# Kernel optimization log

Hardware: AMD Instinct MI355X
Metric: run time of the kernel (lower is better)

Reference implementation:

```python
import jax, jax.numpy as jnp
import numpy as np

TEMPERATURE = 0.07
NORM_EPS = 1e-12  # matches torch F.normalize eps


def setup_inputs() -> dict:
    key = jax.random.key(0)
    k1, k2 = jax.random.split(key)
    emb = jax.random.normal(k1, (4, 256, 61, 61), dtype=jnp.float32)
    targets = jax.random.randint(k2, (4, 61, 61), 0, 5, dtype=jnp.int64)
    return {"emb": emb, "targets": targets}


def reference(emb, targets):
    n, c, h, w = emb.shape
    # (N,C,H,W) -> (N*H*W, C), L2-normalized per pixel
    feats = emb.transpose(0, 2, 3, 1).reshape(-1, c)
    norms = jnp.maximum(jnp.linalg.norm(feats, axis=1, keepdims=True), NORM_EPS)
    feats = feats / norms
    labels = targets.reshape(-1)  # (T,)
    T = labels.shape[0]

    sim = jnp.matmul(feats, feats.T) / TEMPERATURE  # (T,T)
    exp_sim = jnp.exp(sim)

    eye = jnp.eye(T, dtype=bool)
    pos_mask = (labels[None, :] == labels[:, None]) & ~eye  # (T,T) bool

    sum_pos = jnp.sum(jnp.where(pos_mask, exp_sim, 0.0), axis=1)  # (T,)
    sum_all = exp_sim.sum(axis=1) - jnp.exp(jnp.diagonal(sim))    # (T,)

    valid = sum_pos > 0
    # safe log: substitute 1.0 where invalid to avoid -inf/NaN, then mask
    safe_pos = jnp.where(valid, sum_pos, 1.0)
    safe_all = jnp.where(valid, sum_all, 1.0)
    per_row = jnp.where(valid, -(jnp.log(safe_pos) - jnp.log(safe_all)), 0.0)
    loss = per_row.sum() / jnp.maximum(valid.sum(), 1).astype(per_row.dtype)
    return loss
```

## Files before the change

kernel.cpp:

```cpp
#include <hip/hip_runtime.h>
#include <cstdint>
#include <cstddef>

#define T_REAL 14884
#define TPAD   14976
#define CDIM   256
#define HW     3721
#define NTILE  234
#define NRB    117
#define NSLICE 8

static constexpr float SCALE = 20.6099291555566f;

typedef _Float16 f16x8 __attribute__((ext_vector_type(8)));
typedef float    f32x4 __attribute__((ext_vector_type(4)));

#define OFF_FEATS 0u
#define SZ_FEATS  ((unsigned)TPAD * CDIM * 2u)
#define OFF_SUMSQ (OFF_FEATS + SZ_FEATS)
#define OFF_LAB   (OFF_SUMSQ + 65536u)
#define OFF_PART  (OFF_LAB + 65536u)
#define SZ_PART   ((unsigned)NRB * NSLICE * 128u * 2u * 4u)
#define OFF_ACC   (OFF_PART + SZ_PART)

__global__ void k_init(const int* __restrict__ targets, int* __restrict__ labels,
                       _Float16* __restrict__ feats, float* __restrict__ sumsq,
                       float* __restrict__ accum) {
    int t = blockIdx.x * 256 + threadIdx.x;
    if (t == 0) { accum[0] = 0.f; accum[1] = 0.f; }
    if (t < TPAD) {
        labels[t] = (t < T_REAL) ? targets[t] : -1;
        if (t < T_REAL) {
            sumsq[t] = 0.f;
        } else {
            float4 z = make_float4(0.f, 0.f, 0.f, 0.f);
            float4* row = (float4*)(feats + (size_t)t * CDIM);
#pragma unroll
            for (int q = 0; q < 32; ++q) row[q] = z;
        }
    }
}

__global__ void k_norm(const float* __restrict__ emb, float* __restrict__ sumsq) {
    int hw = blockIdx.x * 256 + threadIdx.x;
    int n  = blockIdx.y, cq = blockIdx.z;
    if (hw >= HW) return;
    const float* p = emb + ((size_t)(n * CDIM + cq * 64)) * HW + hw;
    float s = 0.f;
#pragma unroll 16
    for (int c = 0; c < 64; ++c) { float v = p[(size_t)c * HW]; s += v * v; }
    atomicAdd(&sumsq[n * HW + hw], s);
}

__global__ void k_pack(const float* __restrict__ emb, const float* __restrict__ sumsq,
                       _Float16* __restrict__ feats) {
    __shared__ float tile[64][65];
    int tx = threadIdx.x & 63, ty = threadIdx.x >> 6;
    int hw0 = blockIdx.x * 64, c0 = blockIdx.y * 64, n = blockIdx.z;
#pragma unroll
    for (int it = 0; it < 16; ++it) {
        int cl = it * 4 + ty;
        int hw = hw0 + tx;
        float v = 0.f;
        if (hw < HW) v = emb[((size_t)(n * CDIM + c0 + cl)) * HW + hw];
        tile[cl][tx] = v;
    }
    __syncthreads();
#pragma unroll
    for (int it = 0; it < 16; ++it) {
        int pl = it * 4 + ty;
        int hw = hw0 + pl;
        if (hw < HW) {
            int t = n * HW + hw;
            float inv = 1.f / fmaxf(sqrtf(sumsq[t]), 1e-12f);
            feats[(size_t)t * CDIM + c0 + tx] = (_Float16)(tile[tx][pl] * inv);
        }
    }
}

__device__ __forceinline__ void stage_tile(const _Float16* __restrict__ feats, int jbase,
                                           _Float16* bufp, int tid) {
#pragma unroll
    for (int sweep = 0; sweep < 4; ++sweep) {
        int ch = sweep * 512 + tid;
        int j  = ch >> 5;
        int qs = ch & 31;
        int qsrc = qs ^ (j & 7);
        const _Float16* src = feats + ((size_t)(jbase + j)) * CDIM + qsrc * 8;
        __builtin_amdgcn_global_load_lds(
            (const __attribute__((address_space(1))) void*)src,
            (__attribute__((address_space(3))) void*)(bufp + (size_t)ch * 8),
            16, 0, 0);
    }
}

__global__ __launch_bounds__(512, 4) void k_main(const _Float16* __restrict__ feats,
                                                 const int* __restrict__ labels,
                                                 float* __restrict__ partials) {
    __shared__ _Float16 buf[2][64 * 256];
    const int tid  = threadIdx.x;
    const int wave = tid >> 6, lane = tid & 63;
    const int il   = lane & 15, quad = lane >> 4;
    const int rb = blockIdx.x, slice = blockIdx.y;
    const int i = rb * 128 + wave * 16 + il;
    const int lab_i = labels[i];

    f16x8 bfr[8];
    const _Float16* fi = feats + (size_t)i * CDIM;
#pragma unroll
    for (int ks = 0; ks < 8; ++ks)
        bfr[ks] = *reinterpret_cast<const f16x8*>(fi + ks * 32 + quad * 8);

    const int hb = (il >> 2) & 1;
    const int qx = quad ^ (il & 3);
    int lofs[4];
#pragma unroll
    for (int jj = 0; jj < 4; ++jj) lofs[jj] = (jj * 16 + il) * 256 + qx * 8;

    float accA = 0.f, accP = 0.f;

    stage_tile(feats, slice * 64, &buf[0][0], tid);
    int cur = 0;
    for (int jt = slice; jt < NTILE; jt += NSLICE) {
        asm volatile("s_waitcnt vmcnt(0)\n\ts_barrier" ::: "memory");
        int nxt = jt + NSLICE;
        if (nxt < NTILE) stage_tile(feats, nxt * 64, &buf[cur ^ 1][0], tid);

        const _Float16* bufc = &buf[cur][0];
        f32x4 acc[4];
#pragma unroll
        for (int jj = 0; jj < 4; ++jj) acc[jj] = (f32x4){0.f, 0.f, 0.f, 0.f};

#pragma unroll
        for (int ks = 0; ks < 8; ++ks) {
            const int ksx = ks ^ hb;
#pragma unroll
            for (int jj = 0; jj < 4; ++jj) {
                f16x8 a = *reinterpret_cast<const f16x8*>(bufc + lofs[jj] + ksx * 32);
                acc[jj] = __builtin_amdgcn_mfma_f32_16x16x32_f16(a, bfr[ks], acc[jj], 0, 0, 0);
            }
        }

        const int jb = jt * 64;
#pragma unroll
        for (int jj = 0; jj < 4; ++jj) {
            const int4 lj = *reinterpret_cast<const int4*>(&labels[jb + jj * 16 + quad * 4]);
#pragma unroll
            for (int r = 0; r < 4; ++r) {
                int ljr = (r == 0) ? lj.x : (r == 1) ? lj.y : (r == 2) ? lj.z : lj.w;
                float e  = exp2f(acc[jj][r] * SCALE);
                float ev = (ljr >= 0) ? e : 0.f;
                accA += ev;
                accP += (ljr == lab_i) ? ev : 0.f;
            }
        }
        cur ^= 1;
    }

    float nsq = 0.f;
#pragma unroll
    for (int ks = 0; ks < 8; ++ks)
#pragma unroll
        for (int e = 0; e < 8; ++e) { float x = (float)bfr[ks][e]; nsq += x * x; }
    nsq += __shfl_xor(nsq, 16);
    nsq += __shfl_xor(nsq, 32);

    accA += __shfl_xor(accA, 16); accA += __shfl_xor(accA, 32);
    accP += __shfl_xor(accP, 16); accP += __shfl_xor(accP, 32);

    if ((((rb * 2 + (wave >> 2)) & 7)) == slice) {
        float ed = exp2f(nsq * SCALE);
        accA -= ed; accP -= ed;
    }

    if (quad == 0) {
        int idx = ((rb * NSLICE + slice) * 128 + wave * 16 + il) * 2;
        partials[idx]     = accA;
        partials[idx + 1] = accP;
    }
}

__global__ void k_reduce(const float* __restrict__ partials, float* __restrict__ accum) {
    int rb = blockIdx.x;
    int tl = threadIdx.x;
    int t  = rb * 128 + tl;
    float per = 0.f, cnt = 0.f;
    if (t < T_REAL) {
        float sA = 0.f, sP = 0.f;
#pragma unroll
        for (int s = 0; s < NSLICE; ++s) {
            int idx = ((rb * NSLICE + s) * 128 + tl) * 2;
            sA += partials[idx];
            sP += partials[idx + 1];
        }
        if (sP > 0.f) {
            per = logf(sA) - logf(sP);
            cnt = 1.f;
        }
    }
#pragma unroll
    for (int off = 32; off >= 1; off >>= 1) {
        per += __shfl_xor(per, off);
        cnt += __shfl_xor(cnt, off);
    }
    if ((tl & 63) == 0) { atomicAdd(&accum[0], per); atomicAdd(&accum[1], cnt); }
}

__global__ void k_final(const float* __restrict__ accum, float* __restrict__ out) {
    out[0] = accum[0] / fmaxf(accum[1], 1.0f);
}

extern "C" void kernel_launch(void* const* d_in, const int* in_sizes, int n_in,
                              void* d_out, int out_size, void* d_ws, size_t ws_size,
                              hipStream_t stream) {
    const float* emb     = (const float*)d_in[0];
    const int*   targets = (const int*)d_in[1];
    float*       out     = (float*)d_out;
    char*        ws      = (char*)d_ws;

    _Float16* feats    = (_Float16*)(ws + OFF_FEATS);
    float*    sumsq    = (float*)(ws + OFF_SUMSQ);
    int*      labels   = (int*)(ws + OFF_LAB);
    float*    partials = (float*)(ws + OFF_PART);
    float*    accum    = (float*)(ws + OFF_ACC);

    k_init  <<<dim3(59),        dim3(256), 0, stream>>>(targets, labels, feats, sumsq, accum);
    k_norm  <<<dim3(15, 4, 4),  dim3(256), 0, stream>>>(emb, sumsq);
    k_pack  <<<dim3(59, 4, 4),  dim3(256), 0, stream>>>(emb, sumsq, feats);
    k_main  <<<dim3(NRB, NSLICE), dim3(512), 0, stream>>>(feats, labels, partials);
    k_reduce<<<dim3(NRB),       dim3(128), 0, stream>>>(partials, accum);
    k_final <<<dim3(1),         dim3(1),   0, stream>>>(accum, out);
}
```

Baseline: 265.8 us.

## Use 32x32 MFMA 64-row register tiles, fuse norm+pack, fold scale into features

The main kernel switches to 32x32x16 MFMAs, with each wave holding 64 query rows in registers, so each LDS tile is reused across more rows. The padding becomes a multiple of 512, and slices go from 8 to 16. The norm and pack kernels are merged into one prep kernel that computes the sum of squares in LDS, removing the atomics and an extra pass over the embeddings. The sqrt of the temperature/log2e scale is folded into the stored features, and padding columns are no longer masked; their exp(0) contributions are subtracted as a constant in the reduction. The cost is fp16 features with scaled magnitudes and higher register pressure (launch bounds lowered to 2).

```diff
diff --git a/kernel.cpp b/kernel.cpp
--- a/kernel.cpp
+++ b/kernel.cpp
@@ -3,36 +3,42 @@
 #include <cstddef>
 
 #define T_REAL 14884
-#define TPAD   14976
+#define TPAD   15360
 #define CDIM   256
 #define HW     3721
-#define NTILE  234
-#define NRB    117
-#define NSLICE 8
-
-static constexpr float SCALE = 20.6099291555566f;
-
-typedef _Float16 f16x8 __attribute__((ext_vector_type(8)));
-typedef float    f32x4 __attribute__((ext_vector_type(4)));
+#define NRB    30
+#define NCT    240
+#define NSL    16
+#define TPS    15
+#define NPADJ  476.0f
+
+static constexpr float SQRT_SCALE = 4.53981598f;
+
+typedef _Float16 f16x8  __attribute__((ext_vector_type(8)));
+typedef float    f32x16 __attribute__((ext_vector_type(16)));
+
+__device__ __forceinline__ float exp2_fast(float x) {
+#if __has_builtin(__builtin_amdgcn_exp2f)
+    return __builtin_amdgcn_exp2f(x);
+#else
+    return exp2f(x);
+#endif
+}
 
 #define OFF_FEATS 0u
 #define SZ_FEATS  ((unsigned)TPAD * CDIM * 2u)
-#define OFF_SUMSQ (OFF_FEATS + SZ_FEATS)
-#define OFF_LAB   (OFF_SUMSQ + 65536u)
-#define OFF_PART  (OFF_LAB + 65536u)
-#define SZ_PART   ((unsigned)NRB * NSLICE * 128u * 2u * 4u)
+#define OFF_LAB   (OFF_FEATS + SZ_FEATS)
+#define OFF_PART  (OFF_LAB + (unsigned)TPAD * 4u)
+#define SZ_PART   ((unsigned)NRB * NSL * 512u * 8u)
 #define OFF_ACC   (OFF_PART + SZ_PART)
 
 __global__ void k_init(const int* __restrict__ targets, int* __restrict__ labels,
-                       _Float16* __restrict__ feats, float* __restrict__ sumsq,
-                       float* __restrict__ accum) {
+                       _Float16* __restrict__ feats, float* __restrict__ accum) {
     int t = blockIdx.x * 256 + threadIdx.x;
     if (t == 0) { accum[0] = 0.f; accum[1] = 0.f; }
     if (t < TPAD) {
         labels[t] = (t < T_REAL) ? targets[t] : -1;
-        if (t < T_REAL) {
-            sumsq[t] = 0.f;
-        } else {
+        if (t >= T_REAL) {
             float4 z = make_float4(0.f, 0.f, 0.f, 0.f);
             float4* row = (float4*)(feats + (size_t)t * CDIM);
 #pragma unroll
@@ -41,39 +47,38 @@
     }
 }
 
-__global__ void k_norm(const float* __restrict__ emb, float* __restrict__ sumsq) {
-    int hw = blockIdx.x * 256 + threadIdx.x;
-    int n  = blockIdx.y, cq = blockIdx.z;
-    if (hw >= HW) return;
-    const float* p = emb + ((size_t)(n * CDIM + cq * 64)) * HW + hw;
-    float s = 0.f;
-#pragma unroll 16
-    for (int c = 0; c < 64; ++c) { float v = p[(size_t)c * HW]; s += v * v; }
-    atomicAdd(&sumsq[n * HW + hw], s);
-}
-
-__global__ void k_pack(const float* __restrict__ emb, const float* __restrict__ sumsq,
-                       _Float16* __restrict__ feats) {
-    __shared__ float tile[64][65];
-    int tx = threadIdx.x & 63, ty = threadIdx.x >> 6;
-    int hw0 = blockIdx.x * 64, c0 = blockIdx.y * 64, n = blockIdx.z;
-#pragma unroll
-    for (int it = 0; it < 16; ++it) {
-        int cl = it * 4 + ty;
-        int hw = hw0 + tx;
-        float v = 0.f;
-        if (hw < HW) v = emb[((size_t)(n * CDIM + c0 + cl)) * HW + hw];
-        tile[cl][tx] = v;
-    }
+__global__ void k_prep(const float* __restrict__ emb, _Float16* __restrict__ feats) {
+    __shared__ float tile[64][257];
+    __shared__ float sspart[4][64];
+    const int tid = threadIdx.x;
+    const int lane = tid & 63, w = tid >> 6;
+    const int px0 = blockIdx.x * 64, n = blockIdx.y;
+    const int hw = px0 + lane;
+
+    float ssq = 0.f;
+    for (int ci = w; ci < CDIM; ci += 4) {
+        float v = (hw < HW) ? emb[((size_t)(n * CDIM + ci)) * HW + hw] : 0.f;
+        tile[lane][ci] = v;
+        ssq += v * v;
+    }
+    sspart[w][lane] = ssq;
     __syncthreads();
-#pragma unroll
-    for (int it = 0; it < 16; ++it) {
-        int pl = it * 4 + ty;
-        int hw = hw0 + pl;
-        if (hw < HW) {
-            int t = n * HW + hw;
-            float inv = 1.f / fmaxf(sqrtf(sumsq[t]), 1e-12f);
-            feats[(size_t)t * CDIM + c0 + tx] = (_Float16)(tile[tx][pl] * inv);
+
+    const int p = tid >> 2, q = tid & 3;
+    float s = sspart[q][p];
+    s += __shfl_xor(s, 1);
+    s += __shfl_xor(s, 2);
+    float inv = SQRT_SCALE / fmaxf(sqrtf(s), 1e-12f);
+
+    const int hwp = px0 + p;
+    if (hwp < HW) {
+        _Float16* dst = feats + ((size_t)(n * HW + hwp)) * CDIM + q * 64;
+#pragma unroll
+        for (int g = 0; g < 8; ++g) {
+            f16x8 o;
+#pragma unroll
+            for (int e = 0; e < 8; ++e) o[e] = (_Float16)(tile[p][q * 64 + g * 8 + e] * inv);
+            *reinterpret_cast<f16x8*>(dst + g * 8) = o;
         }
     }
 }
@@ -84,9 +89,9 @@
     for (int sweep = 0; sweep < 4; ++sweep) {
         int ch = sweep * 512 + tid;
         int j  = ch >> 5;
-        int qs = ch & 31;
-        int qsrc = qs ^ (j & 7);
-        const _Float16* src = feats + ((size_t)(jbase + j)) * CDIM + qsrc * 8;
+        int c  = ch & 31;
+        int csrc = c ^ (j & 7);
+        const _Float16* src = feats + ((size_t)(jbase + j)) * CDIM + csrc * 8;
         __builtin_amdgcn_global_load_lds(
             (const __attribute__((address_space(1))) void*)src,
             (__attribute__((address_space(3))) void*)(bufp + (size_t)ch * 8),
@@ -94,116 +99,121 @@
     }
 }
 
-__global__ __launch_bounds__(512, 4) void k_main(const _Float16* __restrict__ feats,
+__global__ __launch_bounds__(512, 2) void k_main(const _Float16* __restrict__ feats,
                                                  const int* __restrict__ labels,
-                                                 float* __restrict__ partials) {
+                                                 float2* __restrict__ partials) {
     __shared__ _Float16 buf[2][64 * 256];
     const int tid  = threadIdx.x;
-    const int wave = tid >> 6, lane = tid & 63;
-    const int il   = lane & 15, quad = lane >> 4;
+    const int w    = tid >> 6, lane = tid & 63;
+    const int lo   = lane & 31, hi = lane >> 5, x3 = lane & 7;
     const int rb = blockIdx.x, slice = blockIdx.y;
-    const int i = rb * 128 + wave * 16 + il;
-    const int lab_i = labels[i];
-
-    f16x8 bfr[8];
-    const _Float16* fi = feats + (size_t)i * CDIM;
-#pragma unroll
-    for (int ks = 0; ks < 8; ++ks)
-        bfr[ks] = *reinterpret_cast<const f16x8*>(fi + ks * 32 + quad * 8);
-
-    const int hb = (il >> 2) & 1;
-    const int qx = quad ^ (il & 3);
-    int lofs[4];
-#pragma unroll
-    for (int jj = 0; jj < 4; ++jj) lofs[jj] = (jj * 16 + il) * 256 + qx * 8;
-
-    float accA = 0.f, accP = 0.f;
+    const int ibase = rb * 512 + w * 64;
+
+    const int labi0 = labels[ibase + lo];
+    const int labi1 = labels[ibase + 32 + lo];
+
+    f16x8 b0[16], b1[16];
+    {
+        const f16x8* r0 = (const f16x8*)(feats + (size_t)(ibase + lo) * CDIM + hi * 8);
+        const f16x8* r1 = (const f16x8*)(feats + (size_t)(ibase + 32 + lo) * CDIM + hi * 8);
+#pragma unroll
+        for (int k = 0; k < 16; ++k) { b0[k] = r0[k * 2]; b1[k] = r1[k * 2]; }
+    }
+
+    float accA0 = 0.f, accP0 = 0.f, accA1 = 0.f, accP1 = 0.f;
+    const int rowoff = lo * 256;
 
     stage_tile(feats, slice * 64, &buf[0][0], tid);
     int cur = 0;
-    for (int jt = slice; jt < NTILE; jt += NSLICE) {
+#pragma unroll 1
+    for (int ti = 0; ti < TPS; ++ti) {
+        const int jt = slice + ti * NSL;
         asm volatile("s_waitcnt vmcnt(0)\n\ts_barrier" ::: "memory");
-        int nxt = jt + NSLICE;
-        if (nxt < NTILE) stage_tile(feats, nxt * 64, &buf[cur ^ 1][0], tid);
-
-        const _Float16* bufc = &buf[cur][0];
-        f32x4 acc[4];
-#pragma unroll
-        for (int jj = 0; jj < 4; ++jj) acc[jj] = (f32x4){0.f, 0.f, 0.f, 0.f};
-
-#pragma unroll
-        for (int ks = 0; ks < 8; ++ks) {
-            const int ksx = ks ^ hb;
-#pragma unroll
-            for (int jj = 0; jj < 4; ++jj) {
-                f16x8 a = *reinterpret_cast<const f16x8*>(bufc + lofs[jj] + ksx * 32);
-                acc[jj] = __builtin_amdgcn_mfma_f32_16x16x32_f16(a, bfr[ks], acc[jj], 0, 0, 0);
+        if (ti + 1 < TPS) stage_tile(feats, (jt + NSL) * 64, &buf[cur ^ 1][0], tid);
+
+        const _Float16* bc = &buf[cur][0];
+        f32x16 c00 = {0,0,0,0,0,0,0,0,0,0,0,0,0,0,0,0};
+        f32x16 c01 = c00, c10 = c00, c11 = c00;
+
+#pragma unroll
+        for (int k = 0; k < 16; ++k) {
+            const int co = ((k * 2 + hi) ^ x3) * 8;
+            f16x8 a0 = *reinterpret_cast<const f16x8*>(bc + rowoff + co);
+            f16x8 a1 = *reinterpret_cast<const f16x8*>(bc + 8192 + rowoff + co);
+            c00 = __builtin_amdgcn_mfma_f32_32x32x16_f16(a0, b0[k], c00, 0, 0, 0);
+            c01 = __builtin_amdgcn_mfma_f32_32x32x16_f16(a0, b1[k], c01, 0, 0, 0);
+            c10 = __builtin_amdgcn_mfma_f32_32x32x16_f16(a1, b0[k], c10, 0, 0, 0);
+            c11 = __builtin_amdgcn_mfma_f32_32x32x16_f16(a1, b1[k], c11, 0, 0, 0);
+        }
+
+        const int jb = jt * 64;
+#pragma unroll
+        for (int jg = 0; jg < 2; ++jg) {
+#pragma unroll
+            for (int q = 0; q < 4; ++q) {
+                const int4 lj = *reinterpret_cast<const int4*>(labels + jb + jg * 32 + q * 8 + hi * 4);
+#pragma unroll
+                for (int r = 0; r < 4; ++r) {
+                    const int ljr = (r == 0) ? lj.x : (r == 1) ? lj.y : (r == 2) ? lj.z : lj.w;
+                    float e0 = exp2_fast((jg ? c10 : c00)[q * 4 + r]);
+                    accA0 += e0;
+                    accP0 += (ljr == labi0) ? e0 : 0.f;
+                    float e1 = exp2_fast((jg ? c11 : c01)[q * 4 + r]);
+                    accA1 += e1;
+                    accP1 += (ljr == labi1) ? e1 : 0.f;
+                }
             }
         }
-
-        const int jb = jt * 64;
-#pragma unroll
-        for (int jj = 0; jj < 4; ++jj) {
-            const int4 lj = *reinterpret_cast<const int4*>(&labels[jb + jj * 16 + quad * 4]);
-#pragma unroll
-            for (int r = 0; r < 4; ++r) {
-                int ljr = (r == 0) ? lj.x : (r == 1) ? lj.y : (r == 2) ? lj.z : lj.w;
-                float e  = exp2f(acc[jj][r] * SCALE);
-                float ev = (ljr >= 0) ? e : 0.f;
-                accA += ev;
-                accP += (ljr == lab_i) ? ev : 0.f;
-            }
-        }
         cur ^= 1;
     }
 
-    float nsq = 0.f;
-#pragma unroll
-    for (int ks = 0; ks < 8; ++ks)
-#pragma unroll
-        for (int e = 0; e < 8; ++e) { float x = (float)bfr[ks][e]; nsq += x * x; }
-    nsq += __shfl_xor(nsq, 16);
-    nsq += __shfl_xor(nsq, 32);
-
-    accA += __shfl_xor(accA, 16); accA += __shfl_xor(accA, 32);
-    accP += __shfl_xor(accP, 16); accP += __shfl_xor(accP, 32);
-
-    if ((((rb * 2 + (wave >> 2)) & 7)) == slice) {
-        float ed = exp2f(nsq * SCALE);
-        accA -= ed; accP -= ed;
-    }
-
-    if (quad == 0) {
-        int idx = ((rb * NSLICE + slice) * 128 + wave * 16 + il) * 2;
-        partials[idx]     = accA;
-        partials[idx + 1] = accP;
-    }
-}
-
-__global__ void k_reduce(const float* __restrict__ partials, float* __restrict__ accum) {
-    int rb = blockIdx.x;
-    int tl = threadIdx.x;
-    int t  = rb * 128 + tl;
+    float n0 = 0.f, n1 = 0.f;
+#pragma unroll
+    for (int k = 0; k < 16; ++k)
+#pragma unroll
+        for (int e = 0; e < 8; ++e) {
+            float v0 = (float)b0[k][e]; n0 += v0 * v0;
+            float v1 = (float)b1[k][e]; n1 += v1 * v1;
+        }
+    n0 += __shfl_xor(n0, 32); n1 += __shfl_xor(n1, 32);
+
+    accA0 += __shfl_xor(accA0, 32); accP0 += __shfl_xor(accP0, 32);
+    accA1 += __shfl_xor(accA1, 32); accP1 += __shfl_xor(accP1, 32);
+
+    if (((rb * 8 + w) & (NSL - 1)) == slice) {
+        float e0 = exp2_fast(n0), e1 = exp2_fast(n1);
+        accA0 -= e0; accP0 -= e0;
+        accA1 -= e1; accP1 -= e1;
+    }
+
+    if (hi == 0) {
+        size_t base = ((size_t)(rb * NSL + slice)) * 512 + w * 64;
+        partials[base + lo]      = make_float2(accA0, accP0);
+        partials[base + 32 + lo] = make_float2(accA1, accP1);
+    }
+}
+
+__global__ void k_reduce(const float2* __restrict__ partials, float* __restrict__ accum) {
+    const int rb = blockIdx.x;
+    const int rl = threadIdx.x;
+    const int t  = rb * 512 + rl;
+    float sA = -NPADJ, sP = 0.f;
+#pragma unroll
+    for (int s = 0; s < NSL; ++s) {
+        float2 v = partials[((size_t)(rb * NSL + s)) * 512 + rl];
+        sA += v.x; sP += v.y;
+    }
     float per = 0.f, cnt = 0.f;
-    if (t < T_REAL) {
-        float sA = 0.f, sP = 0.f;
-#pragma unroll
-        for (int s = 0; s < NSLICE; ++s) {
-            int idx = ((rb * NSLICE + s) * 128 + tl) * 2;
-            sA += partials[idx];
-            sP += partials[idx + 1];
-        }
-        if (sP > 0.f) {
-            per = logf(sA) - logf(sP);
-            cnt = 1.f;
-        }
+    if (t < T_REAL && sP > 0.f) {
+        per = logf(sA) - logf(sP);
+        cnt = 1.f;
     }
 #pragma unroll
     for (int off = 32; off >= 1; off >>= 1) {
         per += __shfl_xor(per, off);
         cnt += __shfl_xor(cnt, off);
     }
-    if ((tl & 63) == 0) { atomicAdd(&accum[0], per); atomicAdd(&accum[1], cnt); }
+    if ((threadIdx.x & 63) == 0) { atomicAdd(&accum[0], per); atomicAdd(&accum[1], cnt); }
 }
 
 __global__ void k_final(const float* __restrict__ accum, float* __restrict__ out) {
@@ -219,15 +229,13 @@
     char*        ws      = (char*)d_ws;
 
     _Float16* feats    = (_Float16*)(ws + OFF_FEATS);
-    float*    sumsq    = (float*)(ws + OFF_SUMSQ);
     int*      labels   = (int*)(ws + OFF_LAB);
-    float*    partials = (float*)(ws + OFF_PART);
+    float2*   partials = (float2*)(ws + OFF_PART);
     float*    accum    = (float*)(ws + OFF_ACC);
 
-    k_init  <<<dim3(59),        dim3(256), 0, stream>>>(targets, labels, feats, sumsq, accum);
-    k_norm  <<<dim3(15, 4, 4),  dim3(256), 0, stream>>>(emb, sumsq);
-    k_pack  <<<dim3(59, 4, 4),  dim3(256), 0, stream>>>(emb, sumsq, feats);
-    k_main  <<<dim3(NRB, NSLICE), dim3(512), 0, stream>>>(feats, labels, partials);
-    k_reduce<<<dim3(NRB),       dim3(128), 0, stream>>>(partials, accum);
+    k_init  <<<dim3(60),        dim3(256), 0, stream>>>(targets, labels, feats, accum);
+    k_prep  <<<dim3(59, 4),     dim3(256), 0, stream>>>(emb, feats);
+    k_main  <<<dim3(NRB, NSL),  dim3(512), 0, stream>>>(feats, labels, partials);
+    k_reduce<<<dim3(NRB),       dim3(512), 0, stream>>>(partials, accum);
     k_final <<<dim3(1),         dim3(1),   0, stream>>>(accum, out);
 }
```

Measured after the change: 226.1 us. 1.18x faster.
